# Performance work log

Measured on AMD Instinct MI355X. Metric: run time of the kernel, lower is better.

Reference implementation:

```python
import jax, jax.numpy as jnp
import numpy as np

B = 512        # batch of parallel sequences
TM1 = 64       # T-1 recurrence steps
BELIEF = 2048  # GRU / deterministic belief size
STATE = 256    # stochastic state size
ACTION = 64
HIDDEN = 2048
EMB = 1024     # embedding_size['fusion']
MIN_STD = 0.1


def setup_inputs() -> dict:
    key = jax.random.key(0)
    ks = jax.random.split(key, 16)
    w = lambda k, shape: jax.random.normal(k, shape, dtype=jnp.float32) * 0.02
    return {
        "prev_state": jax.random.normal(ks[0], (B, STATE), dtype=jnp.float32),
        "actions": jax.random.normal(ks[1], (TM1, B, ACTION), dtype=jnp.float32),
        "prev_belief": jax.random.normal(ks[2], (B, BELIEF), dtype=jnp.float32),
        "obs_emb": jax.random.normal(ks[3], (TM1, B, EMB), dtype=jnp.float32),
        "nonterminals": jnp.ones((TM1, B, 1), dtype=jnp.float32),
        # fc_embed_state_action
        "W_embed": w(ks[4], (STATE + ACTION, BELIEF)),
        "b_embed": jnp.zeros((BELIEF,), jnp.float32),
        # GRUCell (input-to-hidden / hidden-to-hidden, gate order r,z,n as torch)
        "Wi": w(ks[5], (BELIEF, 3 * BELIEF)),
        "bi": jnp.zeros((3 * BELIEF,), jnp.float32),
        "Wh": w(ks[6], (BELIEF, 3 * BELIEF)),
        "bh": jnp.zeros((3 * BELIEF,), jnp.float32),
        # stochastic_state_model (prior): h -> hidden -> 2*state
        "W1": w(ks[7], (BELIEF, HIDDEN)),
        "b1": jnp.zeros((HIDDEN,), jnp.float32),
        "W2": w(ks[8], (HIDDEN, 2 * STATE)),
        "b2": jnp.zeros((2 * STATE,), jnp.float32),
        # obs_encoder (posterior): cat(h, obs_emb) -> hidden -> 2*state
        "W1p": w(ks[9], (BELIEF + EMB, HIDDEN)),
        "b1p": jnp.zeros((HIDDEN,), jnp.float32),
        "W2p": w(ks[10], (HIDDEN, 2 * STATE)),
        "b2p": jnp.zeros((2 * STATE,), jnp.float32),
        # reparameterized-sampling noise (rsample = loc + scale * eps)
        "eps_prior": jax.random.normal(ks[11], (TM1, B, STATE), dtype=jnp.float32),
        "eps_post": jax.random.normal(ks[12], (TM1, B, STATE), dtype=jnp.float32),
    }


def reference(prev_state, actions, prev_belief, obs_emb, nonterminals,
              W_embed, b_embed, Wi, bi, Wh, bh,
              W1, b1, W2, b2, W1p, b1p, W2p, b2p,
              eps_prior, eps_post):
    def step(carry, xs):
        belief, post_state = carry
        a, obs, nt, ep, eq = xs
        s = post_state * nt                                   # [B, S]
        hidden = jax.nn.relu(jnp.concatenate([s, a], axis=1) @ W_embed + b_embed)
        # torch.nn.GRUCell math (gate order r, z, n)
        gi = hidden @ Wi + bi
        gh = belief @ Wh + bh
        i_r, i_z, i_n = jnp.split(gi, 3, axis=1)
        h_r, h_z, h_n = jnp.split(gh, 3, axis=1)
        r = jax.nn.sigmoid(i_r + h_r)
        z = jax.nn.sigmoid(i_z + h_z)
        n = jnp.tanh(i_n + r * h_n)
        new_belief = (1.0 - z) * n + z * belief               # [B, H]
        # prior stochastic state model
        hp = jax.nn.relu(new_belief @ W1 + b1)
        loc_p, raw_p = jnp.split(hp @ W2 + b2, 2, axis=1)
        scale_p = jax.nn.softplus(raw_p) + MIN_STD
        prior_state = loc_p + scale_p * ep                    # rsample
        # posterior from obs embedding
        hq = jax.nn.relu(jnp.concatenate([new_belief, obs], axis=1) @ W1p + b1p)
        loc_q, raw_q = jnp.split(hq @ W2p + b2p, 2, axis=1)
        scale_q = jax.nn.softplus(raw_q) + MIN_STD
        post_new = loc_q + scale_q * eq                       # rsample
        ys = (new_belief, prior_state, loc_p, scale_p, post_new, loc_q, scale_q)
        return (new_belief, post_new), ys

    _, ys = jax.lax.scan(step, (prev_belief, prev_state),
                         (actions, obs_emb, nonterminals, eps_prior, eps_post))
    # (beliefs, prior_states, prior_means, prior_std_devs,
    #  posterior_states, posterior_means, posterior_std_devs), each [T-1, B, ...]
    return ys
```

## Files before the change

### kernel.cpp

```cpp
#include <hip/hip_runtime.h>
#include <hip/hip_bf16.h>
#include <cstdint>

typedef __hip_bfloat16 bf16;
typedef __attribute__((ext_vector_type(8))) short bf16x8v;
typedef __attribute__((ext_vector_type(4))) float f32x4;

#define NB 256
#define NT 512
#define TM1 64

#define OUT_BEL  ((size_t)0)
#define OUT_PST  ((size_t)67108864)
#define OUT_PMU  ((size_t)75497472)
#define OUT_PSD  ((size_t)83886080)
#define OUT_QST  ((size_t)92274688)
#define OUT_QMU  ((size_t)100663296)
#define OUT_QSD  ((size_t)109051904)

__device__ __forceinline__ void gload_lds16(const bf16* g, bf16* l) {
  __builtin_amdgcn_global_load_lds(
      (const __attribute__((address_space(1))) unsigned int*)g,
      (__attribute__((address_space(3))) unsigned int*)l, 16, 0, 0);
}

__device__ __forceinline__ unsigned short bfb(float f) {
  bf16 h = __float2bfloat16(f);
  return *reinterpret_cast<unsigned short*>(&h);
}

__device__ __forceinline__ float sigmoidf_(float x) { return 1.f / (1.f + __expf(-x)); }

__device__ __forceinline__ int jid(int bid, int nj) {
  return (bid < nj) ? ((bid & 7) * (nj >> 3) + (bid >> 3)) : -1;
}

__device__ __forceinline__ void gbar(unsigned* bars, unsigned e, int bid) {
  __syncthreads();
  const int g = bid & 7;
  const int tid = threadIdx.x;
  if (tid == 0) {
    __threadfence();
    __hip_atomic_fetch_add(&bars[16 * g], 1u, __ATOMIC_RELAXED, __HIP_MEMORY_SCOPE_AGENT);
  }
  if (bid == 0) {
    if (tid < 8) {
      while (__hip_atomic_load(&bars[16 * tid], __ATOMIC_RELAXED, __HIP_MEMORY_SCOPE_AGENT) < 32u * e)
        __builtin_amdgcn_s_sleep(1);
    }
    __syncthreads();
    if (tid < 8)
      __hip_atomic_store(&bars[128 + 16 * tid], e, __ATOMIC_RELAXED, __HIP_MEMORY_SCOPE_AGENT);
  } else if (tid == 0) {
    while (__hip_atomic_load(&bars[128 + 16 * g], __ATOMIC_RELAXED, __HIP_MEMORY_SCOPE_AGENT) < e)
      __builtin_amdgcn_s_sleep(2);
  }
  if (tid == 0) __threadfence();
  __syncthreads();
}

template<int BM, int BN, int DEPTH>
__device__ void gemm_tile(const bf16* __restrict__ A, const bf16* __restrict__ B,
                          const float* __restrict__ bias, void* __restrict__ C,
                          int N, int K, int nm, int mode, int job, int tid,
                          char* pool)
{
  constexpr int LA = BM * 8 / NT;
  constexpr int LB = BN * 8 / NT;
  constexpr int L = LA + LB;
  constexpr int WMt = BM / 4, WNt = BN / 2;
  constexpr int MR = WMt / 16, NR = WNt / 16;
  bf16* sAb = (bf16*)pool;
  bf16* sBb = (bf16*)(pool + (size_t)DEPTH * BM * 64 * 2);

  const int m0 = (job % nm) * BM;
  const int n0 = (job / nm) * BN;
  const int lane = tid & 63;
  const int wid = tid >> 6;
  const int wm = wid >> 1, wn = wid & 1;
  const int lr = lane & 15;
  const int lg = lane >> 4;

  const bf16* Abase = A + (size_t)m0 * K;
  const bf16* Bbase = B + (size_t)n0 * K;

  auto stage = [&](int buf, int k0) {
    bf16* dA = sAb + buf * (BM * 64);
    bf16* dB = sBb + buf * (BN * 64);
    #pragma unroll
    for (int i = 0; i < LA; ++i) {
      int c = i * NT + tid;
      int row = c >> 3, kc = c & 7;
      gload_lds16(Abase + (size_t)row * K + k0 + ((kc ^ (row & 7)) << 3), &dA[c * 8]);
    }
    #pragma unroll
    for (int i = 0; i < LB; ++i) {
      int c = i * NT + tid;
      int row = c >> 3, kc = c & 7;
      gload_lds16(Bbase + (size_t)row * K + k0 + ((kc ^ (row & 7)) << 3), &dB[c * 8]);
    }
  };

  f32x4 acc[MR][NR] = {};
  __syncthreads();
  const int nk = K >> 6;
  #pragma unroll
  for (int d = 0; d < DEPTH; ++d)
    if (d < nk) stage(d, d << 6);
  int cur = 0;
  for (int it = 0; it < nk; ++it) {
    if (DEPTH == 3) {
      if (it + 2 < nk)      { asm volatile("s_waitcnt vmcnt(%0)" :: "n"(2 * L) : "memory"); }
      else if (it + 1 < nk) { asm volatile("s_waitcnt vmcnt(%0)" :: "n"(L) : "memory"); }
      else                  { asm volatile("s_waitcnt vmcnt(0)" ::: "memory"); }
    } else {
      if (it + 1 < nk)      { asm volatile("s_waitcnt vmcnt(%0)" :: "n"(L) : "memory"); }
      else                  { asm volatile("s_waitcnt vmcnt(0)" ::: "memory"); }
    }
    __builtin_amdgcn_sched_barrier(0);
    __builtin_amdgcn_s_barrier();
    __builtin_amdgcn_sched_barrier(0);
    const bf16* cA = sAb + cur * (BM * 64);
    const bf16* cB = sBb + cur * (BN * 64);
    #pragma unroll
    for (int kk = 0; kk < 2; ++kk) {
      const int jg = kk * 4 + lg;
      bf16x8v af[MR], bfv[NR];
      #pragma unroll
      for (int m = 0; m < MR; ++m) {
        int ar = wm * WMt + m * 16 + lr;
        af[m] = *(const bf16x8v*)&cA[ar * 64 + ((jg ^ (ar & 7)) << 3)];
      }
      #pragma unroll
      for (int n = 0; n < NR; ++n) {
        int br = wn * WNt + n * 16 + lr;
        bfv[n] = *(const bf16x8v*)&cB[br * 64 + ((jg ^ (br & 7)) << 3)];
      }
      #pragma unroll
      for (int m = 0; m < MR; ++m)
        #pragma unroll
        for (int n = 0; n < NR; ++n)
          acc[m][n] = __builtin_amdgcn_mfma_f32_16x16x32_bf16(af[m], bfv[n], acc[m][n], 0, 0, 0);
    }
    __builtin_amdgcn_sched_barrier(0);
    __builtin_amdgcn_s_barrier();
    __builtin_amdgcn_sched_barrier(0);
    if (it + DEPTH < nk) stage(cur, (it + DEPTH) << 6);
    cur = (cur + 1 == DEPTH) ? 0 : cur + 1;
  }

  const int r0 = (lane >> 4) * 4;
  #pragma unroll
  for (int m = 0; m < MR; ++m) {
    #pragma unroll
    for (int n = 0; n < NR; ++n) {
      int gc = n0 + wn * WNt + n * 16 + lr;
      float bv = bias[gc];
      #pragma unroll
      for (int r = 0; r < 4; ++r) {
        int gr = m0 + wm * WMt + m * 16 + r0 + r;
        float v = acc[m][n][r] + bv;
        if (mode == 1)
          ((bf16*)C)[(size_t)gr * N + gc] = __float2bfloat16(v > 0.f ? v : 0.f);
        else
          ((float*)C)[(size_t)gr * N + gc] = v;
      }
    }
  }
}

__device__ void fused_gru(const bf16* __restrict__ hidden, const bf16* __restrict__ belsrc,
                          const bf16* __restrict__ WiT, const bf16* __restrict__ WhT,
                          const float* __restrict__ bi, const float* __restrict__ bh,
                          float* __restrict__ belief_f32, float* __restrict__ out_bel,
                          bf16* __restrict__ belslot,
                          int job, int tid, char* pool)
{
  bf16 (*sA)[64 * 64]  = (bf16(*)[64 * 64])pool;
  bf16 (*sB)[192 * 64] = (bf16(*)[192 * 64])(pool + 16384);

  const int m0 = (job & 7) * 64;
  const int j0 = (job >> 3) * 64;
  const int lane = tid & 63;
  const int wid = tid >> 6;
  const int wm = wid >> 2, wn = wid & 3;
  const int lr = lane & 15;
  const int lg = lane >> 4;

  auto stage = [&](int buf, int gt) {
    const bf16* Ab; const bf16* Bb; int k0;
    if (gt < 32) { Ab = hidden; Bb = WiT; k0 = gt << 6; }
    else         { Ab = belsrc; Bb = WhT; k0 = (gt - 32) << 6; }
    {
      int c = tid;
      int row = c >> 3, kc = c & 7;
      gload_lds16(Ab + (size_t)(m0 + row) * 2048 + k0 + ((kc ^ (row & 7)) << 3),
                  &sA[buf][c * 8]);
    }
    #pragma unroll
    for (int i = 0; i < 3; ++i) {
      int c = i * NT + tid;
      int r = c >> 3, kc = c & 7;
      int grow = (r >> 6) * 2048 + j0 + (r & 63);
      gload_lds16(Bb + (size_t)grow * 2048 + k0 + ((kc ^ (r & 7)) << 3),
                  &sB[buf][c * 8]);
    }
  };

  f32x4 ar_[2] = {}, az_[2] = {}, ain[2] = {}, ahn[2] = {};

  auto body = [&](int gt, f32x4 (&ax)[2]) {
    const int cur = gt & 1;
    if (gt < 63) { asm volatile("s_waitcnt vmcnt(4)" ::: "memory"); }
    else         { asm volatile("s_waitcnt vmcnt(0)" ::: "memory"); }
    __builtin_amdgcn_sched_barrier(0);
    __builtin_amdgcn_s_barrier();
    __builtin_amdgcn_sched_barrier(0);
    #pragma unroll
    for (int kk = 0; kk < 2; ++kk) {
      const int jg = kk * 4 + lg;
      bf16x8v af[2], bg[3];
      #pragma unroll
      for (int m = 0; m < 2; ++m) {
        int arow = wm * 32 + m * 16 + lr;
        af[m] = *(const bf16x8v*)&sA[cur][arow * 64 + ((jg ^ (arow & 7)) << 3)];
      }
      #pragma unroll
      for (int g = 0; g < 3; ++g) {
        int br = g * 64 + wn * 16 + lr;
        bg[g] = *(const bf16x8v*)&sB[cur][br * 64 + ((jg ^ (br & 7)) << 3)];
      }
      #pragma unroll
      for (int m = 0; m < 2; ++m) {
        ar_[m] = __builtin_amdgcn_mfma_f32_16x16x32_bf16(af[m], bg[0], ar_[m], 0, 0, 0);
        az_[m] = __builtin_amdgcn_mfma_f32_16x16x32_bf16(af[m], bg[1], az_[m], 0, 0, 0);
        ax[m]  = __builtin_amdgcn_mfma_f32_16x16x32_bf16(af[m], bg[2], ax[m], 0, 0, 0);
      }
    }
    __builtin_amdgcn_sched_barrier(0);
    __builtin_amdgcn_s_barrier();
    __builtin_amdgcn_sched_barrier(0);
    if (gt + 2 < 64) stage(cur, gt + 2);
  };

  __syncthreads();
  stage(0, 0);
  stage(1, 1);
  for (int gt = 0; gt < 32; ++gt) body(gt, ain);
  for (int gt = 32; gt < 64; ++gt) body(gt, ahn);

  const int gc = j0 + wn * 16 + lr;
  const float br_b  = bi[gc] + bh[gc];
  const float bz_b  = bi[2048 + gc] + bh[2048 + gc];
  const float bin_b = bi[4096 + gc];
  const float bhn_b = bh[4096 + gc];
  const int r0 = (lane >> 4) * 4;
  #pragma unroll
  for (int m = 0; m < 2; ++m) {
    #pragma unroll
    for (int r = 0; r < 4; ++r) {
      int grow = m0 + wm * 32 + m * 16 + r0 + r;
      size_t idx = (size_t)grow * 2048 + gc;
      float rr = sigmoidf_(ar_[m][r] + br_b);
      float zz = sigmoidf_(az_[m][r] + bz_b);
      float nn = tanhf(ain[m][r] + bin_b + rr * (ahn[m][r] + bhn_b));
      float bo = belief_f32[idx];
      float nb = (1.f - zz) * nn + zz * bo;
      belief_f32[idx] = nb;
      out_bel[idx] = nb;
      belslot[idx] = __float2bfloat16(nb);
    }
  }
}

__device__ void gemm_w1p(const bf16* __restrict__ Abel, const bf16* __restrict__ Aobs,
                         const bf16* __restrict__ B, const float* __restrict__ bias,
                         bf16* __restrict__ C, int job, int tid, char* pool)
{
  constexpr int K = 3072, NK = 48;
  bf16* sAb = (bf16*)pool;
  bf16* sBb = (bf16*)(pool + 49152);

  const int m0 = (job & 3) * 128;
  const int n0 = (job >> 2) * 128;
  const int lane = tid & 63;
  const int wid = tid >> 6;
  const int wm = wid >> 1, wn = wid & 1;
  const int lr = lane & 15;
  const int lg = lane >> 4;

  auto stage = [&](int buf, int k0) {
    bf16* dA = sAb + buf * (128 * 64);
    bf16* dB = sBb + buf * (128 * 64);
    #pragma unroll
    for (int i = 0; i < 2; ++i) {
      int c = i * NT + tid;
      int row = c >> 3, kc = c & 7;
      int sw = (kc ^ (row & 7)) << 3;
      const bf16* src = (k0 < 2048)
          ? Abel + (size_t)(m0 + row) * 2048 + k0 + sw
          : Aobs + (size_t)(m0 + row) * 1024 + (k0 - 2048) + sw;
      gload_lds16(src, &dA[c * 8]);
    }
    #pragma unroll
    for (int i = 0; i < 2; ++i) {
      int c = i * NT + tid;
      int row = c >> 3, kc = c & 7;
      gload_lds16(B + (size_t)(n0 + row) * K + k0 + ((kc ^ (row & 7)) << 3), &dB[c * 8]);
    }
  };

  f32x4 acc[2][4] = {};
  __syncthreads();
  stage(0, 0); stage(1, 64); stage(2, 128);
  int cur = 0;
  for (int it = 0; it < NK; ++it) {
    if (it + 2 < NK)      { asm volatile("s_waitcnt vmcnt(8)" ::: "memory"); }
    else if (it + 1 < NK) { asm volatile("s_waitcnt vmcnt(4)" ::: "memory"); }
    else                  { asm volatile("s_waitcnt vmcnt(0)" ::: "memory"); }
    __builtin_amdgcn_sched_barrier(0);
    __builtin_amdgcn_s_barrier();
    __builtin_amdgcn_sched_barrier(0);
    const bf16* cA = sAb + cur * (128 * 64);
    const bf16* cB = sBb + cur * (128 * 64);
    #pragma unroll
    for (int kk = 0; kk < 2; ++kk) {
      const int jg = kk * 4 + lg;
      bf16x8v af[2], bfv[4];
      #pragma unroll
      for (int m = 0; m < 2; ++m) {
        int ar = wm * 32 + m * 16 + lr;
        af[m] = *(const bf16x8v*)&cA[ar * 64 + ((jg ^ (ar & 7)) << 3)];
      }
      #pragma unroll
      for (int n = 0; n < 4; ++n) {
        int br = wn * 64 + n * 16 + lr;
        bfv[n] = *(const bf16x8v*)&cB[br * 64 + ((jg ^ (br & 7)) << 3)];
      }
      #pragma unroll
      for (int m = 0; m < 2; ++m)
        #pragma unroll
        for (int n = 0; n < 4; ++n)
          acc[m][n] = __builtin_amdgcn_mfma_f32_16x16x32_bf16(af[m], bfv[n], acc[m][n], 0, 0, 0);
    }
    __builtin_amdgcn_sched_barrier(0);
    __builtin_amdgcn_s_barrier();
    __builtin_amdgcn_sched_barrier(0);
    if (it + 3 < NK) stage(cur, (it + 3) << 6);
    cur = (cur + 1 == 3) ? 0 : cur + 1;
  }

  const int r0 = (lane >> 4) * 4;
  #pragma unroll
  for (int n = 0; n < 4; ++n) {
    int gcn = n0 + wn * 64 + n * 16 + lr;
    float bv = bias[gcn];
    #pragma unroll
    for (int m = 0; m < 2; ++m)
      #pragma unroll
      for (int r = 0; r < 4; ++r) {
        int gr = m0 + wm * 32 + m * 16 + r0 + r;
        float v = acc[m][n][r] + bv;
        C[(size_t)gr * 2048 + gcn] = __float2bfloat16(v > 0.f ? v : 0.f);
      }
  }
}

__device__ void w2p_tile(const bf16* __restrict__ hq, const bf16* __restrict__ W2pT,
                         const float* __restrict__ b2p, const float* __restrict__ eps,
                         float* __restrict__ o_mu, float* __restrict__ o_sd,
                         float* __restrict__ o_st,
                         const float* __restrict__ nt_next,
                         const float* __restrict__ act_next,
                         bf16* __restrict__ xcat, int make_xcat,
                         int blk, int tid, char* pool)
{
  constexpr int K = 2048, NK = K / 64;
  const int mb = blk & 7, nl = blk >> 3;
  const int m0 = mb * 64;
  const int j0 = nl * 32;

  bf16 (*sA)[64 * 64] = (bf16(*)[64 * 64])pool;
  bf16 (*sB)[64 * 64] = (bf16(*)[64 * 64])(pool + 16384);
  float* tile = (float*)pool;

  const int lane = tid & 63;
  const int wid = tid >> 6;
  const int wm = wid >> 1, wn = wid & 1;
  const int lr = lane & 15;
  const int lg = lane >> 4;

  const bf16* Abase = hq + (size_t)m0 * K;

  auto stage = [&](int buf, int k0) {
    {
      int c = tid;
      int row = c >> 3, kc = c & 7;
      gload_lds16(Abase + (size_t)row * K + k0 + ((kc ^ (row & 7)) << 3), &sA[buf][c * 8]);
    }
    {
      int c = tid;
      int row = c >> 3, kc = c & 7;
      int grow = (row < 32) ? (j0 + row) : (224 + j0 + row);
      gload_lds16(W2pT + (size_t)grow * K + k0 + ((kc ^ (row & 7)) << 3), &sB[buf][c * 8]);
    }
  };

  f32x4 acc[2] = {};
  __syncthreads();
  stage(0, 0);
  stage(1, 64);
  for (int it = 0; it < NK; ++it) {
    const int cur = it & 1;
    if (it + 1 < NK) { asm volatile("s_waitcnt vmcnt(2)" ::: "memory"); }
    else             { asm volatile("s_waitcnt vmcnt(0)" ::: "memory"); }
    __builtin_amdgcn_sched_barrier(0);
    __builtin_amdgcn_s_barrier();
    __builtin_amdgcn_sched_barrier(0);
    #pragma unroll
    for (int kk = 0; kk < 2; ++kk) {
      const int jg = kk * 4 + lg;
      int ar = wm * 16 + lr;
      bf16x8v af = *(const bf16x8v*)&sA[cur][ar * 64 + ((jg ^ (ar & 7)) << 3)];
      #pragma unroll
      for (int n = 0; n < 2; ++n) {
        int br = wn * 32 + n * 16 + lr;
        bf16x8v bfv = *(const bf16x8v*)&sB[cur][br * 64 + ((jg ^ (br & 7)) << 3)];
        acc[n] = __builtin_amdgcn_mfma_f32_16x16x32_bf16(af, bfv, acc[n], 0, 0, 0);
      }
    }
    __builtin_amdgcn_sched_barrier(0);
    __builtin_amdgcn_s_barrier();
    __builtin_amdgcn_sched_barrier(0);
    if (it + 2 < NK) stage(cur, (it + 2) << 6);
  }

  const int r0 = (lane >> 4) * 4;
  #pragma unroll
  for (int n = 0; n < 2; ++n) {
    int tc = wn * 32 + n * 16 + lr;
    #pragma unroll
    for (int r = 0; r < 4; ++r)
      tile[(wm * 16 + r0 + r) * 64 + tc] = acc[n][r];
  }
  __syncthreads();

  for (int e = tid; e < 64 * 32; e += NT) {
    int rr = e >> 5, cc = e & 31;
    int b = m0 + rr;
    int j = j0 + cc;
    float loc = tile[rr * 64 + cc] + b2p[j];
    float raw = tile[rr * 64 + 32 + cc] + b2p[256 + j];
    float sp = (raw > 20.f) ? raw : log1pf(__expf(raw));
    float scale = sp + 0.1f;
    float st = loc + scale * eps[(size_t)b * 256 + j];
    o_mu[(size_t)b * 256 + j] = loc;
    o_sd[(size_t)b * 256 + j] = scale;
    o_st[(size_t)b * 256 + j] = st;
    if (make_xcat)
      xcat[(size_t)b * 320 + j] = __float2bfloat16(st * nt_next[b]);
  }
  if (make_xcat && nl == 0) {
    for (int e = tid; e < 64 * 64; e += NT) {
      int rr = e >> 6, cc = e & 63;
      int b = m0 + rr;
      xcat[(size_t)b * 320 + 256 + cc] = __float2bfloat16(act_next[(size_t)b * 64 + cc]);
    }
  }
}

__device__ void transpose_phase(const float* __restrict__ src, bf16* __restrict__ dst,
                                int K, int N, int bid, int tid, float* t )
{
  const int ntile = (K / 32) * (N / 32);
  const int tx = tid & 31, ty = tid >> 5;
  for (int it = bid; it < ntile; it += NB) {
    int kt = it % (K / 32), nt = it / (K / 32);
    int k0 = kt * 32, n0 = nt * 32;
    __syncthreads();
    #pragma unroll
    for (int i = 0; i < 32; i += 16)
      t[(ty + i) * 33 + tx] = src[(size_t)(k0 + ty + i) * N + n0 + tx];
    __syncthreads();
    #pragma unroll
    for (int i = 0; i < 32; i += 16)
      dst[(size_t)(n0 + ty + i) * K + k0 + tx] = __float2bfloat16(t[tx * 33 + ty + i]);
  }
}

struct Args {
  const float *prev_state, *actions, *prev_belief, *obs_emb, *nonterm;
  const float *W_embed, *b_embed, *Wi, *bi, *Wh, *bh;
  const float *W1, *b1, *W2, *b2, *W1p, *b1p, *W2p, *b2p;
  const float *eps_p, *eps_q;
  bf16 *WembT, *WiT, *WhT, *W1T, *W2T, *W1pT, *W2pT;
  float* belief_f32; bf16 *bel_init, *xcat, *hidden, *obsB;
  bf16 *hq, *belA, *hp; float* yp;
  float* out;
  unsigned* cnt;
};

__global__ __launch_bounds__(NT, 2) void mega(Args a)
{
  extern __shared__ char pool[];
  const int bid = blockIdx.x;
  const int tid = threadIdx.x;
  const int sj = ((bid & 7) << 5) | (bid >> 3);
  unsigned ep = 0;

  transpose_phase(a.W_embed, a.WembT, 320, 2048, bid, tid, (float*)pool);
  transpose_phase(a.Wi,  a.WiT,  2048, 6144, bid, tid, (float*)pool);
  transpose_phase(a.Wh,  a.WhT,  2048, 6144, bid, tid, (float*)pool);
  transpose_phase(a.W1,  a.W1T,  2048, 2048, bid, tid, (float*)pool);
  transpose_phase(a.W2,  a.W2T,  2048, 512,  bid, tid, (float*)pool);
  transpose_phase(a.W1p, a.W1pT, 3072, 2048, bid, tid, (float*)pool);
  transpose_phase(a.W2p, a.W2pT, 2048, 512,  bid, tid, (float*)pool);
  for (int i = bid * NT + tid; i < 512 * 2048; i += NB * NT) {
    float v = a.prev_belief[i];
    a.belief_f32[i] = v;
    a.bel_init[i] = __float2bfloat16(v);
  }
  for (int i = bid * NT + tid; i < 512 * 320; i += NB * NT) {
    int b = i / 320, c = i - b * 320;
    float v = (c < 256) ? a.prev_state[b * 256 + c] * a.nonterm[b]
                        : a.actions[b * 64 + (c - 256)];
    a.xcat[i] = __float2bfloat16(v);
  }
  for (int i = bid * NT + tid; i < TM1 * 512 * 1024 / 4; i += NB * NT) {
    float4 v = *(const float4*)&a.obs_emb[(size_t)i * 4];
    ushort4 u; u.x = bfb(v.x); u.y = bfb(v.y); u.z = bfb(v.z); u.w = bfb(v.w);
    *(ushort4*)&a.obsB[(size_t)i * 4] = u;
  }
  gbar(a.cnt, ++ep, bid);

  gemm_tile<64, 64, 2>(a.xcat, a.WembT, a.b_embed, a.hidden, 2048, 320, 8, 1, sj, tid, pool);
  gbar(a.cnt, ++ep, bid);

  for (int t = 0; t < TM1; ++t) {
    const bf16* belsrc = (t == 0) ? a.bel_init : a.belA + (size_t)(t - 1) * 512 * 2048;
    fused_gru(a.hidden, belsrc, a.WiT, a.WhT, a.bi, a.bh,
              a.belief_f32,
              a.out + OUT_BEL + (size_t)t * 512 * 2048,
              a.belA + (size_t)t * 512 * 2048,
              sj, tid, pool);
    gbar(a.cnt, ++ep, bid);

    {
      int j = jid(bid, 64);
      if (j >= 0)
        gemm_w1p(a.belA + (size_t)t * 512 * 2048,
                 a.obsB + (size_t)t * 512 * 1024,
                 a.W1pT, a.b1p, a.hq, j, tid, pool);
    }
    gbar(a.cnt, ++ep, bid);

    {
      int tn = (t < TM1 - 1) ? t + 1 : t;
      if (bid < 64) {
        w2p_tile(a.hq, a.W2pT, a.b2p,
                 a.eps_q + (size_t)t * 512 * 256,
                 a.out + OUT_QMU + (size_t)t * 512 * 256,
                 a.out + OUT_QSD + (size_t)t * 512 * 256,
                 a.out + OUT_QST + (size_t)t * 512 * 256,
                 a.nonterm + (size_t)tn * 512,
                 a.actions + (size_t)tn * 512 * 64,
                 a.xcat, (t < TM1 - 1) ? 1 : 0, bid, tid, pool);
      } else if (t >= 8) {
        const int fc = (t >> 3) - 1;
        const int q  = t & 7;
        const int fb = bid - 64;
        const bf16* Ach = a.belA + (size_t)fc * 4096 * 2048;
        if (q < 2) {
          gemm_tile<128, 128, 2>(Ach, a.W1T, a.b1, a.hp, 2048, 2048, 32, 1,
                                 q * 192 + fb, tid, pool);
        } else if (q == 2) {
          if (fb < 128)
            gemm_tile<128, 128, 2>(Ach, a.W1T, a.b1, a.hp, 2048, 2048, 32, 1,
                                   384 + fb, tid, pool);
        } else if (q == 3) {
          if (fb < 128)
            gemm_tile<128, 128, 2>(a.hp, a.W2T, a.b2, a.yp, 512, 2048, 32, 0,
                                   fb, tid, pool);
        } else if (q == 4) {
          for (int i = fb * NT + tid; i < 4096 * 256; i += 192 * NT) {
            int r = i >> 8, j = i & 255;
            float loc = a.yp[(size_t)r * 512 + j];
            float raw = a.yp[(size_t)r * 512 + 256 + j];
            float sp = (raw > 20.f) ? raw : log1pf(__expf(raw));
            float scale = sp + 0.1f;
            size_t o = (size_t)fc * 4096 * 256 + i;
            a.out[OUT_PMU + o] = loc;
            a.out[OUT_PSD + o] = scale;
            a.out[OUT_PST + o] = loc + scale * a.eps_p[o];
          }
        }
      }
    }
    gbar(a.cnt, ++ep, bid);

    if (t < TM1 - 1) {
      gemm_tile<64, 64, 2>(a.xcat, a.WembT, a.b_embed, a.hidden, 2048, 320, 8, 1, sj, tid, pool);
      gbar(a.cnt, ++ep, bid);
    }
  }

  {
    const bf16* Ach = a.belA + (size_t)7 * 4096 * 2048;
    gemm_tile<128, 128, 2>(Ach, a.W1T, a.b1, a.hp, 2048, 2048, 32, 1, sj, tid, pool);
    gemm_tile<128, 128, 2>(Ach, a.W1T, a.b1, a.hp, 2048, 2048, 32, 1, sj + 256, tid, pool);
    gbar(a.cnt, ++ep, bid);

    if (sj < 128)
      gemm_tile<128, 128, 2>(a.hp, a.W2T, a.b2, a.yp, 512, 2048, 32, 0, sj, tid, pool);
    gbar(a.cnt, ++ep, bid);

    for (int i = bid * NT + tid; i < 4096 * 256; i += NB * NT) {
      int r = i >> 8, j = i & 255;
      float loc = a.yp[(size_t)r * 512 + j];
      float raw = a.yp[(size_t)r * 512 + 256 + j];
      float sp = (raw > 20.f) ? raw : log1pf(__expf(raw));
      float scale = sp + 0.1f;
      size_t o = (size_t)7 * 4096 * 256 + i;
      a.out[OUT_PMU + o] = loc;
      a.out[OUT_PSD + o] = scale;
      a.out[OUT_PST + o] = loc + scale * a.eps_p[o];
    }
    gbar(a.cnt, ++ep, bid);
  }
}

extern "C" void kernel_launch(void* const* d_in, const int* in_sizes, int n_in,
                              void* d_out, int out_size, void* d_ws, size_t ws_size,
                              hipStream_t stream)
{
  (void)in_sizes; (void)n_in; (void)out_size; (void)ws_size;
  Args a;
  a.prev_state = (const float*)d_in[0];
  a.actions    = (const float*)d_in[1];
  a.prev_belief= (const float*)d_in[2];
  a.obs_emb    = (const float*)d_in[3];
  a.nonterm    = (const float*)d_in[4];
  a.W_embed    = (const float*)d_in[5];
  a.b_embed    = (const float*)d_in[6];
  a.Wi         = (const float*)d_in[7];
  a.bi         = (const float*)d_in[8];
  a.Wh         = (const float*)d_in[9];
  a.bh         = (const float*)d_in[10];
  a.W1         = (const float*)d_in[11];
  a.b1         = (const float*)d_in[12];
  a.W2         = (const float*)d_in[13];
  a.b2         = (const float*)d_in[14];
  a.W1p        = (const float*)d_in[15];
  a.b1p        = (const float*)d_in[16];
  a.W2p        = (const float*)d_in[17];
  a.b2p        = (const float*)d_in[18];
  a.eps_p      = (const float*)d_in[19];
  a.eps_q      = (const float*)d_in[20];
  a.out        = (float*)d_out;

  char* ws = (char*)d_ws;
  size_t off = 0;
  auto alloc = [&](size_t bytes) -> char* {
    char* p = ws + off;
    off = (off + bytes + 255) & ~(size_t)255;
    return p;
  };
  a.cnt        = (unsigned*)alloc(4096);
  a.WembT      = (bf16*)alloc((size_t)2048 * 320 * 2);
  a.WiT        = (bf16*)alloc((size_t)6144 * 2048 * 2);
  a.WhT        = (bf16*)alloc((size_t)6144 * 2048 * 2);
  a.W1T        = (bf16*)alloc((size_t)2048 * 2048 * 2);
  a.W2T        = (bf16*)alloc((size_t)512 * 2048 * 2);
  a.W1pT       = (bf16*)alloc((size_t)2048 * 3072 * 2);
  a.W2pT       = (bf16*)alloc((size_t)512 * 2048 * 2);
  a.belief_f32 = (float*)alloc((size_t)512 * 2048 * 4);
  a.bel_init   = (bf16*)alloc((size_t)512 * 2048 * 2);
  a.xcat       = (bf16*)alloc((size_t)512 * 320 * 2);
  a.hidden     = (bf16*)alloc((size_t)512 * 2048 * 2);
  a.obsB       = (bf16*)alloc((size_t)TM1 * 512 * 1024 * 2);
  a.hq         = (bf16*)alloc((size_t)512 * 2048 * 2);
  a.belA       = (bf16*)alloc((size_t)TM1 * 512 * 2048 * 2);
  a.hp         = (bf16*)alloc((size_t)4096 * 2048 * 2);
  a.yp         = (float*)alloc((size_t)4096 * 512 * 4);

  hipFuncSetAttribute((const void*)mega,
                      hipFuncAttributeMaxDynamicSharedMemorySize, 98304);
  hipMemsetAsync(a.cnt, 0, 4096, stream);
  mega<<<NB, NT, 98304, stream>>>(a);
}
```

Measured before the change: 10.24 ms.

## Triple-buffer GRU tile loads and spread W1p GEMM across all blocks

The fused GRU step moves from double to triple buffering in LDS, prefetching three k-tiles ahead with adjusted vmcnt waits to hide more global load latency. The posterior W1p GEMM shrinks its tile from 128x128 to 64x64, so it runs as 256 jobs over all persistent blocks instead of 64. The aim is to raise parallelism in that per-step phase that had left most CUs idle. In exchange, the smaller tiles give less operand reuse per block and fetch more global traffic, and the GRU buffers use more LDS.

```diff
diff --git a/kernel.cpp b/kernel.cpp
--- a/kernel.cpp
+++ b/kernel.cpp
@@ -177,7 +177,7 @@
                           int job, int tid, char* pool)
 {
   bf16 (*sA)[64 * 64]  = (bf16(*)[64 * 64])pool;
-  bf16 (*sB)[192 * 64] = (bf16(*)[192 * 64])(pool + 16384);
+  bf16 (*sB)[192 * 64] = (bf16(*)[192 * 64])(pool + 24576);
 
   const int m0 = (job & 7) * 64;
   const int j0 = (job >> 3) * 64;
@@ -208,11 +208,12 @@
   };
 
   f32x4 ar_[2] = {}, az_[2] = {}, ain[2] = {}, ahn[2] = {};
+  int cur = 0;
 
   auto body = [&](int gt, f32x4 (&ax)[2]) {
-    const int cur = gt & 1;
-    if (gt < 63) { asm volatile("s_waitcnt vmcnt(4)" ::: "memory"); }
-    else         { asm volatile("s_waitcnt vmcnt(0)" ::: "memory"); }
+    if (gt < 62)      { asm volatile("s_waitcnt vmcnt(8)" ::: "memory"); }
+    else if (gt == 62){ asm volatile("s_waitcnt vmcnt(4)" ::: "memory"); }
+    else              { asm volatile("s_waitcnt vmcnt(0)" ::: "memory"); }
     __builtin_amdgcn_sched_barrier(0);
     __builtin_amdgcn_s_barrier();
     __builtin_amdgcn_sched_barrier(0);
@@ -240,12 +241,14 @@
     __builtin_amdgcn_sched_barrier(0);
     __builtin_amdgcn_s_barrier();
     __builtin_amdgcn_sched_barrier(0);
-    if (gt + 2 < 64) stage(cur, gt + 2);
+    if (gt + 3 < 64) stage(cur, gt + 3);
+    cur = (cur + 1 == 3) ? 0 : cur + 1;
   };
 
   __syncthreads();
   stage(0, 0);
   stage(1, 1);
+  stage(2, 2);
   for (int gt = 0; gt < 32; ++gt) body(gt, ain);
   for (int gt = 32; gt < 64; ++gt) body(gt, ahn);
 
@@ -278,11 +281,11 @@
                          bf16* __restrict__ C, int job, int tid, char* pool)
 {
   constexpr int K = 3072, NK = 48;
-  bf16* sAb = (bf16*)pool;
-  bf16* sBb = (bf16*)(pool + 49152);
-
-  const int m0 = (job & 3) * 128;
-  const int n0 = (job >> 2) * 128;
+  bf16 (*sA)[64 * 64] = (bf16(*)[64 * 64])pool;
+  bf16 (*sB)[64 * 64] = (bf16(*)[64 * 64])(pool + 24576);
+
+  const int m0 = (job & 7) * 64;
+  const int n0 = (job >> 3) * 64;
   const int lane = tid & 63;
   const int wid = tid >> 6;
   const int wm = wid >> 1, wn = wid & 1;
@@ -290,58 +293,44 @@
   const int lg = lane >> 4;
 
   auto stage = [&](int buf, int k0) {
-    bf16* dA = sAb + buf * (128 * 64);
-    bf16* dB = sBb + buf * (128 * 64);
-    #pragma unroll
-    for (int i = 0; i < 2; ++i) {
-      int c = i * NT + tid;
+    {
+      int c = tid;
       int row = c >> 3, kc = c & 7;
       int sw = (kc ^ (row & 7)) << 3;
       const bf16* src = (k0 < 2048)
           ? Abel + (size_t)(m0 + row) * 2048 + k0 + sw
           : Aobs + (size_t)(m0 + row) * 1024 + (k0 - 2048) + sw;
-      gload_lds16(src, &dA[c * 8]);
-    }
-    #pragma unroll
-    for (int i = 0; i < 2; ++i) {
-      int c = i * NT + tid;
+      gload_lds16(src, &sA[buf][c * 8]);
+    }
+    {
+      int c = tid;
       int row = c >> 3, kc = c & 7;
-      gload_lds16(B + (size_t)(n0 + row) * K + k0 + ((kc ^ (row & 7)) << 3), &dB[c * 8]);
+      gload_lds16(B + (size_t)(n0 + row) * K + k0 + ((kc ^ (row & 7)) << 3), &sB[buf][c * 8]);
     }
   };
 
-  f32x4 acc[2][4] = {};
+  f32x4 acc[2] = {};
   __syncthreads();
   stage(0, 0); stage(1, 64); stage(2, 128);
   int cur = 0;
   for (int it = 0; it < NK; ++it) {
-    if (it + 2 < NK)      { asm volatile("s_waitcnt vmcnt(8)" ::: "memory"); }
-    else if (it + 1 < NK) { asm volatile("s_waitcnt vmcnt(4)" ::: "memory"); }
+    if (it + 2 < NK)      { asm volatile("s_waitcnt vmcnt(4)" ::: "memory"); }
+    else if (it + 1 < NK) { asm volatile("s_waitcnt vmcnt(2)" ::: "memory"); }
     else                  { asm volatile("s_waitcnt vmcnt(0)" ::: "memory"); }
     __builtin_amdgcn_sched_barrier(0);
     __builtin_amdgcn_s_barrier();
     __builtin_amdgcn_sched_barrier(0);
-    const bf16* cA = sAb + cur * (128 * 64);
-    const bf16* cB = sBb + cur * (128 * 64);
     #pragma unroll
     for (int kk = 0; kk < 2; ++kk) {
       const int jg = kk * 4 + lg;
-      bf16x8v af[2], bfv[4];
-      #pragma unroll
-      for (int m = 0; m < 2; ++m) {
-        int ar = wm * 32 + m * 16 + lr;
-        af[m] = *(const bf16x8v*)&cA[ar * 64 + ((jg ^ (ar & 7)) << 3)];
-      }
-      #pragma unroll
-      for (int n = 0; n < 4; ++n) {
-        int br = wn * 64 + n * 16 + lr;
-        bfv[n] = *(const bf16x8v*)&cB[br * 64 + ((jg ^ (br & 7)) << 3)];
-      }
-      #pragma unroll
-      for (int m = 0; m < 2; ++m)
-        #pragma unroll
-        for (int n = 0; n < 4; ++n)
-          acc[m][n] = __builtin_amdgcn_mfma_f32_16x16x32_bf16(af[m], bfv[n], acc[m][n], 0, 0, 0);
+      int arow = wm * 16 + lr;
+      bf16x8v af = *(const bf16x8v*)&sA[cur][arow * 64 + ((jg ^ (arow & 7)) << 3)];
+      #pragma unroll
+      for (int n = 0; n < 2; ++n) {
+        int br = wn * 32 + n * 16 + lr;
+        bf16x8v bv = *(const bf16x8v*)&sB[cur][br * 64 + ((jg ^ (br & 7)) << 3)];
+        acc[n] = __builtin_amdgcn_mfma_f32_16x16x32_bf16(af, bv, acc[n], 0, 0, 0);
+      }
     }
     __builtin_amdgcn_sched_barrier(0);
     __builtin_amdgcn_s_barrier();
@@ -352,17 +341,15 @@
 
   const int r0 = (lane >> 4) * 4;
   #pragma unroll
-  for (int n = 0; n < 4; ++n) {
-    int gcn = n0 + wn * 64 + n * 16 + lr;
+  for (int n = 0; n < 2; ++n) {
+    int gcn = n0 + wn * 32 + n * 16 + lr;
     float bv = bias[gcn];
     #pragma unroll
-    for (int m = 0; m < 2; ++m)
-      #pragma unroll
-      for (int r = 0; r < 4; ++r) {
-        int gr = m0 + wm * 32 + m * 16 + r0 + r;
-        float v = acc[m][n][r] + bv;
-        C[(size_t)gr * 2048 + gcn] = __float2bfloat16(v > 0.f ? v : 0.f);
-      }
+    for (int r = 0; r < 4; ++r) {
+      int gr = m0 + wm * 16 + r0 + r;
+      float v = acc[n][r] + bv;
+      C[(size_t)gr * 2048 + gcn] = __float2bfloat16(v > 0.f ? v : 0.f);
+    }
   }
 }
 
@@ -545,13 +532,9 @@
               sj, tid, pool);
     gbar(a.cnt, ++ep, bid);
 
-    {
-      int j = jid(bid, 64);
-      if (j >= 0)
-        gemm_w1p(a.belA + (size_t)t * 512 * 2048,
-                 a.obsB + (size_t)t * 512 * 1024,
-                 a.W1pT, a.b1p, a.hq, j, tid, pool);
-    }
+    gemm_w1p(a.belA + (size_t)t * 512 * 2048,
+             a.obsB + (size_t)t * 512 * 1024,
+             a.W1pT, a.b1p, a.hq, sj, tid, pool);
     gbar(a.cnt, ++ep, bid);
 
     {
```

Result: faster. 8.937 ms (-12.7%).
